# Kernel optimization log

Measured on AMD Instinct MI355X. Metric: run time of the kernel, lower is better.

The kernel has to match this reference:

```python
import jax, jax.numpy as jnp
import numpy as np

DIM = 768
NUM_HEADS = 8
HEAD_DIM = DIM // NUM_HEADS
SCALE = HEAD_DIM ** -0.5


def setup_inputs() -> dict:
    key = jax.random.key(0)
    k1, k2, k3, k4 = jax.random.split(key, 4)
    B, C, H, W = 8, DIM, 32, 32
    x = jax.random.normal(k1, (B, C, H, W), dtype=jnp.float32)
    # torch Linear stores weight as (out, in); y = x @ W.T + b
    w_qkv = jax.random.normal(k2, (3 * DIM, DIM), dtype=jnp.float32) * (DIM ** -0.5)
    w_proj = jax.random.normal(k3, (DIM, DIM), dtype=jnp.float32) * (DIM ** -0.5)
    b_proj = jax.random.normal(k4, (DIM,), dtype=jnp.float32) * 0.02
    return {"x": x, "w_qkv": w_qkv, "w_proj": w_proj, "b_proj": b_proj}


def reference(x, w_qkv, w_proj, b_proj):
    B, C, H, W = x.shape
    N = H * W
    nh, hd = NUM_HEADS, HEAD_DIM
    # (B, C, H, W) -> (B, N, C)
    tokens = x.reshape(B, C, N).transpose(0, 2, 1)
    qkv = tokens @ w_qkv.T  # (B, N, 3C), no bias (qkv_bias=False)
    qkv = qkv.reshape(B, N, 3, nh, hd).transpose(2, 0, 3, 1, 4)  # (3, B, nh, N, hd)
    q, k, v = qkv[0], qkv[1], qkv[2]
    attn = jnp.einsum('bhnd,bhmd->bhnm', q, k) * SCALE
    attn = jax.nn.softmax(attn, axis=-1)  # attn_drop=0.0 (eval)
    out = jnp.einsum('bhnm,bhmd->bhnd', attn, v)  # (B, nh, N, hd)
    out = out.transpose(0, 2, 1, 3).reshape(B, N, C)
    out = out @ w_proj.T + b_proj  # proj_drop=0.0
    return out.transpose(0, 2, 1).reshape(B, C, H, W)
```

## Files before the change

kernel.cpp:

```cpp
#include <hip/hip_runtime.h>

typedef short s16x8 __attribute__((ext_vector_type(8)));
typedef short s16x4 __attribute__((ext_vector_type(4)));
typedef float f32x4 __attribute__((ext_vector_type(4)));
typedef int   i32x4 __attribute__((ext_vector_type(4)));
typedef unsigned u32x2 __attribute__((ext_vector_type(2)));

#define SCALE_F 0.10206207261596577f
#define KLOG2E  0.14724444f
#define FIXM    12.0f

__device__ __forceinline__ unsigned short f2bf(float f) {
  unsigned u = __builtin_bit_cast(unsigned, f);
  u += 0x7fffu + ((u >> 16) & 1u);
  return (unsigned short)(u >> 16);
}
__device__ __forceinline__ unsigned cvt_pk_bf16(float a, float b) {
  unsigned r;
  asm("v_cvt_pk_bf16_f32 %0, %1, %2" : "=v"(r) : "v"(a), "v"(b));
  return r;
}
__device__ __forceinline__ float exp2_fast(float x) {
  float r;
  asm("v_exp_f32 %0, %1" : "=v"(r) : "v"(x));
  return r;
}

#define MFMA16(a, b, c) __builtin_amdgcn_mfma_f32_16x16x32_bf16((a), (b), (c), 0, 0, 0)

__device__ __forceinline__ void gl_lds16(const unsigned short* g, unsigned short* l) {
  __builtin_amdgcn_global_load_lds(
      (const __attribute__((address_space(1))) void*)g,
      (__attribute__((address_space(3))) void*)l, 16, 0, 0);
}

__global__ __launch_bounds__(256) void cvt_bf16_kernel(const float* __restrict__ src,
                                                       unsigned short* __restrict__ dst, int n4) {
  int i = blockIdx.x * 256 + threadIdx.x;
  if (i >= n4) return;
  f32x4 v = reinterpret_cast<const f32x4*>(src)[i];
  s16x4 o;
  o[0] = (short)f2bf(v[0]); o[1] = (short)f2bf(v[1]);
  o[2] = (short)f2bf(v[2]); o[3] = (short)f2bf(v[3]);
  reinterpret_cast<s16x4*>(dst)[i] = o;
}

__global__ __launch_bounds__(256) void transpose_x_kernel(const float* __restrict__ x,
                                                          unsigned short* __restrict__ tokens) {
  __shared__ float t[32][33];
  const int ct = blockIdx.x * 32, nt = blockIdx.y * 32, b = blockIdx.z;
  const int tx = threadIdx.x, ty = threadIdx.y;
  const float* xp = x + (size_t)b * 768 * 1024;
#pragma unroll
  for (int r = 0; r < 4; ++r) {
    int c = ty + r * 8;
    t[c][tx] = xp[(size_t)(ct + c) * 1024 + nt + tx];
  }
  __syncthreads();
  unsigned short* tp = tokens + (size_t)b * 1024 * 768;
#pragma unroll
  for (int r = 0; r < 4; ++r) {
    int n = ty + r * 8;
    tp[(size_t)(nt + n) * 768 + ct + tx] = f2bf(t[tx][n]);
  }
}

__global__ __launch_bounds__(512, 4) void qkv_gemm_kernel(const unsigned short* __restrict__ A,
                                                          const unsigned short* __restrict__ Bt,
                                                          unsigned short* __restrict__ Qo,
                                                          unsigned short* __restrict__ Ko,
                                                          unsigned short* __restrict__ Vt) {
  __shared__ unsigned short lds[36864];
  const int tid = threadIdx.x;
  const int wave = tid >> 6, lane = tid & 63;
  const int wm = wave >> 1, wn = wave & 1;
  const int lr = lane & 15, lg = lane >> 4;
  const int bid = blockIdx.x;
  const int xcd = bid & 7, idx = bid >> 3;
  const int m0 = (xcd * 4 + idx / 18) * 256;
  const int n0 = (idx % 18) * 128;

  const int srow = tid >> 2, sslot = tid & 3;

  f32x4 acc[4][4] = {};

#define STAGE_KT(ktv, bb)                                                       \
  {                                                                             \
    unsigned short* lb = lds + (bb) * 12288;                                    \
    _Pragma("unroll")                                                           \
    for (int rr = 0; rr < 2; ++rr) {                                            \
      const int row = rr * 128 + srow;                                          \
      const int c = sslot ^ ((row >> 1) & 3);                                   \
      gl_lds16(A + (size_t)(m0 + row) * 768 + (ktv) * 32 + c * 8,               \
               lb + rr * 4096 + wave * 512);                                    \
    }                                                                           \
    {                                                                           \
      const int c = sslot ^ ((srow >> 1) & 3);                                  \
      gl_lds16(Bt + (size_t)(n0 + srow) * 768 + (ktv) * 32 + c * 8,             \
               lb + 8192 + wave * 512);                                         \
    }                                                                           \
  }

  STAGE_KT(0, 0)
  STAGE_KT(1, 1)
  asm volatile("s_waitcnt vmcnt(3)" ::: "memory");
  __builtin_amdgcn_s_barrier();

  int cb = 0;
  for (int kt = 0; kt < 24; ++kt) {
    unsigned short* curb = lds + cb * 12288;
    if (kt < 22) {
      const int sb = (cb == 0) ? 2 : cb - 1;
      STAGE_KT(kt + 2, sb)
    }
    s16x8 af[4], bf[4];
#pragma unroll
    for (int mi = 0; mi < 4; ++mi) {
      const int row = wm * 64 + mi * 16 + lr;
      af[mi] = *reinterpret_cast<const s16x8*>(
          &curb[row * 32 + ((lg ^ ((row >> 1) & 3)) * 8)]);
    }
#pragma unroll
    for (int ni = 0; ni < 4; ++ni) {
      const int row = wn * 64 + ni * 16 + lr;
      bf[ni] = *reinterpret_cast<const s16x8*>(
          &curb[8192 + row * 32 + ((lg ^ ((row >> 1) & 3)) * 8)]);
    }
#pragma unroll
    for (int mi = 0; mi < 4; ++mi)
#pragma unroll
      for (int ni = 0; ni < 4; ++ni)
        acc[mi][ni] = MFMA16(af[mi], bf[ni], acc[mi][ni]);
    asm volatile("s_waitcnt lgkmcnt(0)" ::: "memory");
    if (kt < 22) {
      asm volatile("s_waitcnt vmcnt(3)" ::: "memory");
    } else if (kt == 22) {
      asm volatile("s_waitcnt vmcnt(0)" ::: "memory");
    }
    __builtin_amdgcn_s_barrier();
    cb = (cb == 2) ? 0 : cb + 1;
  }
#undef STAGE_KT

  const int colbase = n0 + wn * 64;
  const int ttype = colbase / 768;
  if (ttype == 2) {
#pragma unroll
    for (int ni = 0; ni < 4; ++ni) {
      const int cc = colbase + ni * 16 + lr - 2 * 768;
      const int h = cc / 96, d = cc - h * 96;
#pragma unroll
      for (int mi = 0; mi < 4; ++mi) {
        const int gm = m0 + wm * 64 + mi * 16 + lg * 4;
        const int b = gm >> 10, n = gm & 1023;
        const int np = (n & ~31) | (((n >> 2) & 3) << 3) | (((n >> 4) & 1) << 2);
        u32x2 p2;
        p2[0] = cvt_pk_bf16(acc[mi][ni][0], acc[mi][ni][1]);
        p2[1] = cvt_pk_bf16(acc[mi][ni][2], acc[mi][ni][3]);
        *reinterpret_cast<s16x4*>(Vt + ((size_t)(b * 8 + h) * 96 + d) * 1024 + np) =
            __builtin_bit_cast(s16x4, p2);
      }
    }
  } else {
    unsigned short* W = lds + wave * 4096;
    unsigned short* dstbuf = (ttype == 0) ? Qo : Ko;
#pragma unroll
    for (int mi = 0; mi < 4; ++mi)
#pragma unroll
      for (int ni = 0; ni < 4; ++ni) {
        const int cc = ni * 16 + lr;
        const int ch = cc >> 3, wi = cc & 7;
#pragma unroll
        for (int j = 0; j < 4; ++j) {
          const int r = mi * 16 + lg * 4 + j;
          W[r * 64 + ((ch ^ (r & 7)) * 8) + wi] = f2bf(acc[mi][ni][j]);
        }
      }
    asm volatile("s_waitcnt lgkmcnt(0)" ::: "memory");
    __builtin_amdgcn_sched_barrier(0);
#pragma unroll
    for (int i = 0; i < 8; ++i) {
      const int r = i * 8 + (lane >> 3), c = lane & 7;
      s16x8 v8 = *reinterpret_cast<const s16x8*>(&W[r * 64 + ((c ^ (r & 7)) * 8)]);
      const int cc = colbase + c * 8 - ttype * 768;
      const int h = cc / 96, d = cc - h * 96;
      const int gm = m0 + wm * 64 + r;
      const int b = gm >> 10, n = gm & 1023;
      *reinterpret_cast<s16x8*>(dstbuf + ((size_t)(b * 8 + h) * 1024 + n) * 96 + d) = v8;
    }
  }
}

__global__ __launch_bounds__(256, 4) void proj_gemm_kernel(const unsigned short* __restrict__ A,
                                                           const unsigned short* __restrict__ Bt,
                                                           const float* __restrict__ bias,
                                                           float* __restrict__ out) {
  __shared__ unsigned short lds[24576];
  const int tid = threadIdx.x;
  const int wave = tid >> 6, lane = tid & 63;
  const int wr = wave >> 1, wc = wave & 1;
  const int lr = lane & 15, lg = lane >> 4;
  const int bid = blockIdx.x;
  const int xcd = bid & 7, idx = bid >> 3;
  const int m0 = (xcd * 8 + idx / 6) * 128;
  const int n0 = (idx % 6) * 128;

  const int r2 = tid >> 2, ss = tid & 3;

  f32x4 acc[4][4] = {};

#define STAGE_P(ktv, bb)                                                        \
  {                                                                             \
    unsigned short* lb = lds + (bb) * 8192;                                     \
    _Pragma("unroll")                                                           \
    for (int i = 0; i < 2; ++i) {                                               \
      const int row = i * 64 + r2;                                              \
      const int c = ss ^ ((row >> 1) & 3);                                      \
      gl_lds16(A + (size_t)(m0 + row) * 768 + (ktv) * 32 + c * 8,               \
               lb + i * 2048 + wave * 512);                                     \
      gl_lds16(Bt + (size_t)(n0 + row) * 768 + (ktv) * 32 + c * 8,              \
               lb + 4096 + i * 2048 + wave * 512);                              \
    }                                                                           \
  }

  STAGE_P(0, 0)
  STAGE_P(1, 1)
  asm volatile("s_waitcnt vmcnt(4)" ::: "memory");
  __builtin_amdgcn_s_barrier();

  int cb = 0;
  for (int kt = 0; kt < 24; ++kt) {
    unsigned short* curb = lds + cb * 8192;
    if (kt < 22) {
      const int sb = (cb == 0) ? 2 : cb - 1;
      STAGE_P(kt + 2, sb)
    }
    s16x8 af[4], bf[4];
#pragma unroll
    for (int mi = 0; mi < 4; ++mi) {
      const int row = wr * 64 + mi * 16 + lr;
      af[mi] = *reinterpret_cast<const s16x8*>(
          &curb[row * 32 + ((lg ^ ((row >> 1) & 3)) * 8)]);
    }
#pragma unroll
    for (int ni = 0; ni < 4; ++ni) {
      const int row = wc * 64 + ni * 16 + lr;
      bf[ni] = *reinterpret_cast<const s16x8*>(
          &curb[4096 + row * 32 + ((lg ^ ((row >> 1) & 3)) * 8)]);
    }
#pragma unroll
    for (int mi = 0; mi < 4; ++mi)
#pragma unroll
      for (int ni = 0; ni < 4; ++ni)
        acc[mi][ni] = MFMA16(af[mi], bf[ni], acc[mi][ni]);
    asm volatile("s_waitcnt lgkmcnt(0)" ::: "memory");
    if (kt < 22) {
      asm volatile("s_waitcnt vmcnt(4)" ::: "memory");
    } else if (kt == 22) {
      asm volatile("s_waitcnt vmcnt(0)" ::: "memory");
    }
    __builtin_amdgcn_s_barrier();
    cb = (cb == 2) ? 0 : cb + 1;
  }
#undef STAGE_P

#pragma unroll
  for (int ni = 0; ni < 4; ++ni) {
    const int col = n0 + wc * 64 + ni * 16 + lr;
    const float bv = bias[col];
#pragma unroll
    for (int mi = 0; mi < 4; ++mi) {
      const int gm = m0 + wr * 64 + mi * 16 + lg * 4;
      const int b = gm >> 10, n = gm & 1023;
      f32x4 v;
#pragma unroll
      for (int j = 0; j < 4; ++j) v[j] = acc[mi][ni][j] + bv;
      *reinterpret_cast<f32x4*>(out + (size_t)b * 768 * 1024 + (size_t)col * 1024 + n) = v;
    }
  }
}

__global__ __launch_bounds__(256, 2) void attn_kernel(const unsigned short* __restrict__ Q,
                                                      const unsigned short* __restrict__ K,
                                                      const unsigned short* __restrict__ Vt,
                                                      unsigned short* __restrict__ Ao) {
  __shared__ unsigned short lds[3][12288];

  const int f = blockIdx.x;
  const int xcd = f & 7;
  const int g = (f >> 3) + xcd * 64;
  const int bh = g >> 3, qb = g & 7;

  const int tid = threadIdx.x, wave = tid >> 6, lane = tid & 63;
  const int lr = lane & 15, lg = lane >> 4;
  const int klo = (lr >> 1) & 3;

  const unsigned short* Qp = Q + (size_t)bh * 1024 * 96;
  const unsigned short* Kp = K + (size_t)bh * 1024 * 96;
  const unsigned short* Vp = Vt + (size_t)bh * 96 * 1024;

  s16x8 qreg[3][2];
#pragma unroll
  for (int u = 0; u < 2; ++u) {
    const int qrow = qb * 128 + wave * 32 + u * 16 + lr;
#pragma unroll
    for (int kd = 0; kd < 3; ++kd)
      qreg[kd][u] = *reinterpret_cast<const s16x8*>(Qp + (size_t)qrow * 96 + kd * 32 + lg * 8);
  }

  float l_lane[2] = {0.f, 0.f};
  f32x4 oacc[6][2] = {};

#define STAGE(bufi, kv0)                                                              \
  {                                                                                   \
    _Pragma("unroll")                                                                 \
    for (int i = 0; i < 6; ++i) {                                                     \
      const int wl = wave + 4 * i;                                                    \
      if (wl < 12) {                                                                  \
        const int kd = wl >> 2, rg = wl & 3;                                          \
        const int row = rg * 16 + (lane >> 2);                                        \
        const int c8 = (lane & 3) ^ ((row >> 1) & 3);                                 \
        gl_lds16(Kp + (size_t)((kv0) + row) * 96 + kd * 32 + c8 * 8,                  \
                 &lds[bufi][0] + kd * 2048 + rg * 512);                               \
      } else {                                                                        \
        const int v = wl - 12;                                                        \
        const int gs = v / 6, rg = v - gs * 6;                                        \
        const int drow = rg * 16 + (lane >> 2);                                       \
        const int c8 = (lane & 3) ^ ((drow >> 1) & 3);                                \
        gl_lds16(Vp + (size_t)drow * 1024 + (kv0) + gs * 32 + c8 * 8,                 \
                 &lds[bufi][0] + 6144 + gs * 3072 + rg * 512);                        \
      }                                                                               \
    }                                                                                 \
  }

  STAGE(0, 0);
  STAGE(1, 64);
  asm volatile("s_waitcnt vmcnt(6)" ::: "memory");
  __builtin_amdgcn_s_barrier();

  int buf = 0;
  for (int gt = 0; gt < 16; ++gt) {
    if (gt < 14) {
      const int sb = (buf == 0) ? 2 : buf - 1;
      STAGE(sb, (gt + 2) * 64);
    }

    f32x4 sacc[4][2] = {};
    __builtin_amdgcn_s_setprio(1);
#pragma unroll
    for (int c = 0; c < 4; ++c) {
      s16x8 kf[3];
#pragma unroll
      for (int kd = 0; kd < 3; ++kd)
        kf[kd] = *reinterpret_cast<const s16x8*>(
            &lds[buf][kd * 2048 + (c * 16 + lr) * 32 + ((lg ^ klo) * 8)]);
#pragma unroll
      for (int kd = 0; kd < 3; ++kd)
#pragma unroll
        for (int u = 0; u < 2; ++u)
          sacc[c][u] = MFMA16(kf[kd], qreg[kd][u], sacc[c][u]);
    }
    __builtin_amdgcn_s_setprio(0);

    unsigned pk[2][4][2];
#pragma unroll
    for (int u = 0; u < 2; ++u) {
      float ts = 0.f;
#pragma unroll
      for (int c = 0; c < 4; ++c) {
        float p0 = exp2_fast(__builtin_fmaf(sacc[c][u][0], KLOG2E, -FIXM));
        float p1 = exp2_fast(__builtin_fmaf(sacc[c][u][1], KLOG2E, -FIXM));
        float p2 = exp2_fast(__builtin_fmaf(sacc[c][u][2], KLOG2E, -FIXM));
        float p3 = exp2_fast(__builtin_fmaf(sacc[c][u][3], KLOG2E, -FIXM));
        ts += (p0 + p1) + (p2 + p3);
        pk[u][c][0] = cvt_pk_bf16(p0, p1);
        pk[u][c][1] = cvt_pk_bf16(p2, p3);
      }
      l_lane[u] += ts;
    }

    __builtin_amdgcn_s_setprio(1);
#pragma unroll
    for (int gs = 0; gs < 2; ++gs) {
      s16x8 pf[2];
#pragma unroll
      for (int u = 0; u < 2; ++u) {
        i32x4 bi;
        bi[0] = (int)pk[u][2 * gs][0];
        bi[1] = (int)pk[u][2 * gs][1];
        bi[2] = (int)pk[u][2 * gs + 1][0];
        bi[3] = (int)pk[u][2 * gs + 1][1];
        pf[u] = __builtin_bit_cast(s16x8, bi);
      }
#pragma unroll
      for (int dt = 0; dt < 6; ++dt) {
        s16x8 vf = *reinterpret_cast<const s16x8*>(
            &lds[buf][6144 + gs * 3072 + (dt * 16 + lr) * 32 + ((lg ^ klo) * 8)]);
#pragma unroll
        for (int u = 0; u < 2; ++u)
          oacc[dt][u] = MFMA16(vf, pf[u], oacc[dt][u]);
      }
    }
    __builtin_amdgcn_s_setprio(0);

    if (gt < 14) {
      asm volatile("s_waitcnt lgkmcnt(0)" ::: "memory");
      asm volatile("s_waitcnt vmcnt(6)" ::: "memory");
      __builtin_amdgcn_s_barrier();
    } else if (gt == 14) {
      asm volatile("s_waitcnt lgkmcnt(0)" ::: "memory");
      asm volatile("s_waitcnt vmcnt(0)" ::: "memory");
      __builtin_amdgcn_s_barrier();
    }
    buf = (buf == 2) ? 0 : buf + 1;
  }

  const int b_ = bh >> 3, h_ = bh & 7;
#pragma unroll
  for (int u = 0; u < 2; ++u) {
    float lt = l_lane[u];
    lt += __shfl_xor(lt, 16);
    lt += __shfl_xor(lt, 32);
    const float invl = 1.0f / lt;
    const int qrow = qb * 128 + wave * 32 + u * 16 + lr;
    unsigned short* orow = Ao + (size_t)(b_ * 1024 + qrow) * 768 + h_ * 96;
#pragma unroll
    for (int dt = 0; dt < 6; ++dt) {
      u32x2 p2;
      p2[0] = cvt_pk_bf16(oacc[dt][u][0] * invl, oacc[dt][u][1] * invl);
      p2[1] = cvt_pk_bf16(oacc[dt][u][2] * invl, oacc[dt][u][3] * invl);
      *reinterpret_cast<s16x4*>(orow + dt * 16 + lg * 4) = __builtin_bit_cast(s16x4, p2);
    }
  }
#undef STAGE
}

extern "C" void kernel_launch(void* const* d_in, const int* in_sizes, int n_in,
                              void* d_out, int out_size, void* d_ws, size_t ws_size,
                              hipStream_t stream) {
  const float* x = (const float*)d_in[0];
  const float* wqkv = (const float*)d_in[1];
  const float* wproj = (const float*)d_in[2];
  const float* bproj = (const float*)d_in[3];
  float* out = (float*)d_out;

  unsigned short* ws = (unsigned short*)d_ws;
  unsigned short* tokens = ws;
  unsigned short* wqkv_b = tokens + 8192 * 768;
  unsigned short* wproj_b = wqkv_b + 2304 * 768;
  unsigned short* Qb = wproj_b + 768 * 768;
  unsigned short* Kb = Qb + 64 * 1024 * 96;
  unsigned short* Vb = Kb + 64 * 1024 * 96;
  unsigned short* Ab = Vb + 64 * 1024 * 96;

  cvt_bf16_kernel<<<1728, 256, 0, stream>>>(wqkv, wqkv_b, 2304 * 768 / 4);
  cvt_bf16_kernel<<<576, 256, 0, stream>>>(wproj, wproj_b, 768 * 768 / 4);
  transpose_x_kernel<<<dim3(24, 32, 8), dim3(32, 8), 0, stream>>>(x, tokens);
  qkv_gemm_kernel<<<576, 512, 0, stream>>>(tokens, wqkv_b, Qb, Kb, Vb);
  attn_kernel<<<512, 256, 0, stream>>>(Qb, Kb, Vb, Ab);
  proj_gemm_kernel<<<384, 256, 0, stream>>>(Ab, wproj_b, bproj, out);
}
```

Before: 111.5 us.

## Halve attention query tile, double-buffer KV, merge weight casts, vectorize transpose

The attention kernel now gives each block 64 query rows (16 per wave) instead of 128, launching twice as many blocks. It also moves from triple to double buffering and raises occupancy to 3 blocks per CU. The two weight-conversion launches are merged into one kernel using packed bf16 conversion, and the input transpose now writes 16-byte vectors over 64-channel tiles. The smaller query tile halves reuse of each K/V tile loaded into LDS, and the shallower prefetch with full barriers exposes more load latency, in exchange for better occupancy and fewer launches.

Result: slower. 115.8 us (+3.9%).

```diff
diff --git a/kernel.cpp b/kernel.cpp
--- a/kernel.cpp
+++ b/kernel.cpp
@@ -34,35 +34,50 @@
       (__attribute__((address_space(3))) void*)l, 16, 0, 0);
 }
 
-__global__ __launch_bounds__(256) void cvt_bf16_kernel(const float* __restrict__ src,
-                                                       unsigned short* __restrict__ dst, int n4) {
+__global__ __launch_bounds__(256) void cvt2_bf16_kernel(const float* __restrict__ s0,
+                                                        unsigned short* __restrict__ d0, int n40,
+                                                        const float* __restrict__ s1,
+                                                        unsigned short* __restrict__ d1, int n41) {
   int i = blockIdx.x * 256 + threadIdx.x;
-  if (i >= n4) return;
+  const float* src;
+  unsigned short* dst;
+  if (i < n40) {
+    src = s0; dst = d0;
+  } else {
+    i -= n40;
+    if (i >= n41) return;
+    src = s1; dst = d1;
+  }
   f32x4 v = reinterpret_cast<const f32x4*>(src)[i];
-  s16x4 o;
-  o[0] = (short)f2bf(v[0]); o[1] = (short)f2bf(v[1]);
-  o[2] = (short)f2bf(v[2]); o[3] = (short)f2bf(v[3]);
-  reinterpret_cast<s16x4*>(dst)[i] = o;
+  u32x2 p;
+  p[0] = cvt_pk_bf16(v[0], v[1]);
+  p[1] = cvt_pk_bf16(v[2], v[3]);
+  reinterpret_cast<s16x4*>(dst)[i] = __builtin_bit_cast(s16x4, p);
 }
 
 __global__ __launch_bounds__(256) void transpose_x_kernel(const float* __restrict__ x,
                                                           unsigned short* __restrict__ tokens) {
-  __shared__ float t[32][33];
-  const int ct = blockIdx.x * 32, nt = blockIdx.y * 32, b = blockIdx.z;
-  const int tx = threadIdx.x, ty = threadIdx.y;
+  __shared__ float t[64][33];
+  const int ct = blockIdx.x * 64, nt = blockIdx.y * 32, b = blockIdx.z;
+  const int tid = threadIdx.x;
+  const int tx = tid & 31, ty = tid >> 5;
   const float* xp = x + (size_t)b * 768 * 1024;
 #pragma unroll
-  for (int r = 0; r < 4; ++r) {
-    int c = ty + r * 8;
+  for (int r = 0; r < 8; ++r) {
+    const int c = ty * 8 + r;
     t[c][tx] = xp[(size_t)(ct + c) * 1024 + nt + tx];
   }
   __syncthreads();
-  unsigned short* tp = tokens + (size_t)b * 1024 * 768;
-#pragma unroll
-  for (int r = 0; r < 4; ++r) {
-    int n = ty + r * 8;
-    tp[(size_t)(nt + n) * 768 + ct + tx] = f2bf(t[tx][n]);
-  }
+  const int n = tid >> 3, cg = tid & 7;
+  u32x2 lo, hi;
+  lo[0] = cvt_pk_bf16(t[cg * 8 + 0][n], t[cg * 8 + 1][n]);
+  lo[1] = cvt_pk_bf16(t[cg * 8 + 2][n], t[cg * 8 + 3][n]);
+  hi[0] = cvt_pk_bf16(t[cg * 8 + 4][n], t[cg * 8 + 5][n]);
+  hi[1] = cvt_pk_bf16(t[cg * 8 + 6][n], t[cg * 8 + 7][n]);
+  i32x4 v;
+  v[0] = (int)lo[0]; v[1] = (int)lo[1]; v[2] = (int)hi[0]; v[3] = (int)hi[1];
+  unsigned short* tp = tokens + (size_t)b * 1024 * 768 + (size_t)(nt + n) * 768 + ct + cg * 8;
+  *reinterpret_cast<i32x4*>(tp) = v;
 }
 
 __global__ __launch_bounds__(512, 4) void qkv_gemm_kernel(const unsigned short* __restrict__ A,
@@ -280,16 +295,16 @@
   }
 }
 
-__global__ __launch_bounds__(256, 2) void attn_kernel(const unsigned short* __restrict__ Q,
+__global__ __launch_bounds__(256, 3) void attn_kernel(const unsigned short* __restrict__ Q,
                                                       const unsigned short* __restrict__ K,
                                                       const unsigned short* __restrict__ Vt,
                                                       unsigned short* __restrict__ Ao) {
-  __shared__ unsigned short lds[3][12288];
+  __shared__ unsigned short lds[2][12288];
 
   const int f = blockIdx.x;
   const int xcd = f & 7;
-  const int g = (f >> 3) + xcd * 64;
-  const int bh = g >> 3, qb = g & 7;
+  const int g = (f >> 3) + xcd * 128;
+  const int bh = g >> 4, qb = g & 15;
 
   const int tid = threadIdx.x, wave = tid >> 6, lane = tid & 63;
   const int lr = lane & 15, lg = lane >> 4;
@@ -299,17 +314,14 @@
   const unsigned short* Kp = K + (size_t)bh * 1024 * 96;
   const unsigned short* Vp = Vt + (size_t)bh * 96 * 1024;
 
-  s16x8 qreg[3][2];
-#pragma unroll
-  for (int u = 0; u < 2; ++u) {
-    const int qrow = qb * 128 + wave * 32 + u * 16 + lr;
-#pragma unroll
-    for (int kd = 0; kd < 3; ++kd)
-      qreg[kd][u] = *reinterpret_cast<const s16x8*>(Qp + (size_t)qrow * 96 + kd * 32 + lg * 8);
-  }
-
-  float l_lane[2] = {0.f, 0.f};
-  f32x4 oacc[6][2] = {};
+  const int qrow = qb * 64 + wave * 16 + lr;
+  s16x8 qreg[3];
+#pragma unroll
+  for (int kd = 0; kd < 3; ++kd)
+    qreg[kd] = *reinterpret_cast<const s16x8*>(Qp + (size_t)qrow * 96 + kd * 32 + lg * 8);
+
+  float l_lane = 0.f;
+  f32x4 oacc[6] = {};
 
 #define STAGE(bufi, kv0)                                                              \
   {                                                                                   \
@@ -334,103 +346,73 @@
   }
 
   STAGE(0, 0);
-  STAGE(1, 64);
-  asm volatile("s_waitcnt vmcnt(6)" ::: "memory");
-  __builtin_amdgcn_s_barrier();
-
-  int buf = 0;
+  __syncthreads();
+
   for (int gt = 0; gt < 16; ++gt) {
-    if (gt < 14) {
-      const int sb = (buf == 0) ? 2 : buf - 1;
-      STAGE(sb, (gt + 2) * 64);
-    }
-
-    f32x4 sacc[4][2] = {};
+    const int buf = gt & 1;
+    if (gt < 15) STAGE(buf ^ 1, (gt + 1) * 64);
+
+    f32x4 sacc[4] = {};
     __builtin_amdgcn_s_setprio(1);
 #pragma unroll
     for (int c = 0; c < 4; ++c) {
-      s16x8 kf[3];
-#pragma unroll
-      for (int kd = 0; kd < 3; ++kd)
-        kf[kd] = *reinterpret_cast<const s16x8*>(
+#pragma unroll
+      for (int kd = 0; kd < 3; ++kd) {
+        s16x8 kf = *reinterpret_cast<const s16x8*>(
             &lds[buf][kd * 2048 + (c * 16 + lr) * 32 + ((lg ^ klo) * 8)]);
-#pragma unroll
-      for (int kd = 0; kd < 3; ++kd)
-#pragma unroll
-        for (int u = 0; u < 2; ++u)
-          sacc[c][u] = MFMA16(kf[kd], qreg[kd][u], sacc[c][u]);
+        sacc[c] = MFMA16(kf, qreg[kd], sacc[c]);
+      }
     }
     __builtin_amdgcn_s_setprio(0);
 
-    unsigned pk[2][4][2];
-#pragma unroll
-    for (int u = 0; u < 2; ++u) {
+    unsigned pk[4][2];
+    {
       float ts = 0.f;
 #pragma unroll
       for (int c = 0; c < 4; ++c) {
-        float p0 = exp2_fast(__builtin_fmaf(sacc[c][u][0], KLOG2E, -FIXM));
-        float p1 = exp2_fast(__builtin_fmaf(sacc[c][u][1], KLOG2E, -FIXM));
-        float p2 = exp2_fast(__builtin_fmaf(sacc[c][u][2], KLOG2E, -FIXM));
-        float p3 = exp2_fast(__builtin_fmaf(sacc[c][u][3], KLOG2E, -FIXM));
+        float p0 = exp2_fast(__builtin_fmaf(sacc[c][0], KLOG2E, -FIXM));
+        float p1 = exp2_fast(__builtin_fmaf(sacc[c][1], KLOG2E, -FIXM));
+        float p2 = exp2_fast(__builtin_fmaf(sacc[c][2], KLOG2E, -FIXM));
+        float p3 = exp2_fast(__builtin_fmaf(sacc[c][3], KLOG2E, -FIXM));
         ts += (p0 + p1) + (p2 + p3);
-        pk[u][c][0] = cvt_pk_bf16(p0, p1);
-        pk[u][c][1] = cvt_pk_bf16(p2, p3);
+        pk[c][0] = cvt_pk_bf16(p0, p1);
+        pk[c][1] = cvt_pk_bf16(p2, p3);
       }
-      l_lane[u] += ts;
+      l_lane += ts;
     }
 
     __builtin_amdgcn_s_setprio(1);
 #pragma unroll
     for (int gs = 0; gs < 2; ++gs) {
-      s16x8 pf[2];
-#pragma unroll
-      for (int u = 0; u < 2; ++u) {
-        i32x4 bi;
-        bi[0] = (int)pk[u][2 * gs][0];
-        bi[1] = (int)pk[u][2 * gs][1];
-        bi[2] = (int)pk[u][2 * gs + 1][0];
-        bi[3] = (int)pk[u][2 * gs + 1][1];
-        pf[u] = __builtin_bit_cast(s16x8, bi);
-      }
+      i32x4 bi;
+      bi[0] = (int)pk[2 * gs][0];
+      bi[1] = (int)pk[2 * gs][1];
+      bi[2] = (int)pk[2 * gs + 1][0];
+      bi[3] = (int)pk[2 * gs + 1][1];
+      s16x8 pf = __builtin_bit_cast(s16x8, bi);
 #pragma unroll
       for (int dt = 0; dt < 6; ++dt) {
         s16x8 vf = *reinterpret_cast<const s16x8*>(
             &lds[buf][6144 + gs * 3072 + (dt * 16 + lr) * 32 + ((lg ^ klo) * 8)]);
-#pragma unroll
-        for (int u = 0; u < 2; ++u)
-          oacc[dt][u] = MFMA16(vf, pf[u], oacc[dt][u]);
+        oacc[dt] = MFMA16(vf, pf, oacc[dt]);
       }
     }
     __builtin_amdgcn_s_setprio(0);
-
-    if (gt < 14) {
-      asm volatile("s_waitcnt lgkmcnt(0)" ::: "memory");
-      asm volatile("s_waitcnt vmcnt(6)" ::: "memory");
-      __builtin_amdgcn_s_barrier();
-    } else if (gt == 14) {
-      asm volatile("s_waitcnt lgkmcnt(0)" ::: "memory");
-      asm volatile("s_waitcnt vmcnt(0)" ::: "memory");
-      __builtin_amdgcn_s_barrier();
-    }
-    buf = (buf == 2) ? 0 : buf + 1;
-  }
-
+    __syncthreads();
+  }
+
+  float lt = l_lane;
+  lt += __shfl_xor(lt, 16);
+  lt += __shfl_xor(lt, 32);
+  const float invl = 1.0f / lt;
   const int b_ = bh >> 3, h_ = bh & 7;
-#pragma unroll
-  for (int u = 0; u < 2; ++u) {
-    float lt = l_lane[u];
-    lt += __shfl_xor(lt, 16);
-    lt += __shfl_xor(lt, 32);
-    const float invl = 1.0f / lt;
-    const int qrow = qb * 128 + wave * 32 + u * 16 + lr;
-    unsigned short* orow = Ao + (size_t)(b_ * 1024 + qrow) * 768 + h_ * 96;
-#pragma unroll
-    for (int dt = 0; dt < 6; ++dt) {
-      u32x2 p2;
-      p2[0] = cvt_pk_bf16(oacc[dt][u][0] * invl, oacc[dt][u][1] * invl);
-      p2[1] = cvt_pk_bf16(oacc[dt][u][2] * invl, oacc[dt][u][3] * invl);
-      *reinterpret_cast<s16x4*>(orow + dt * 16 + lg * 4) = __builtin_bit_cast(s16x4, p2);
-    }
+  unsigned short* orow = Ao + (size_t)(b_ * 1024 + qrow) * 768 + h_ * 96;
+#pragma unroll
+  for (int dt = 0; dt < 6; ++dt) {
+    u32x2 p2;
+    p2[0] = cvt_pk_bf16(oacc[dt][0] * invl, oacc[dt][1] * invl);
+    p2[1] = cvt_pk_bf16(oacc[dt][2] * invl, oacc[dt][3] * invl);
+    *reinterpret_cast<s16x4*>(orow + dt * 16 + lg * 4) = __builtin_bit_cast(s16x4, p2);
   }
 #undef STAGE
 }
@@ -453,10 +435,10 @@
   unsigned short* Vb = Kb + 64 * 1024 * 96;
   unsigned short* Ab = Vb + 64 * 1024 * 96;
 
-  cvt_bf16_kernel<<<1728, 256, 0, stream>>>(wqkv, wqkv_b, 2304 * 768 / 4);
-  cvt_bf16_kernel<<<576, 256, 0, stream>>>(wproj, wproj_b, 768 * 768 / 4);
-  transpose_x_kernel<<<dim3(24, 32, 8), dim3(32, 8), 0, stream>>>(x, tokens);
+  cvt2_bf16_kernel<<<2304, 256, 0, stream>>>(wqkv, wqkv_b, 2304 * 768 / 4,
+                                             wproj, wproj_b, 768 * 768 / 4);
+  transpose_x_kernel<<<dim3(12, 32, 8), 256, 0, stream>>>(x, tokens);
   qkv_gemm_kernel<<<576, 512, 0, stream>>>(tokens, wqkv_b, Qb, Kb, Vb);
-  attn_kernel<<<512, 256, 0, stream>>>(Qb, Kb, Vb, Ab);
+  attn_kernel<<<1024, 256, 0, stream>>>(Qb, Kb, Vb, Ab);
   proj_gemm_kernel<<<384, 256, 0, stream>>>(Ab, wproj_b, bproj, out);
 }
```

## Merge weight conversions, widen transpose stores, shrink QKV GEMM tiles to 128x128

Applied to the files above, without the earlier changes.

The two fp32-to-bf16 weight conversion launches are merged into one kernel that uses packed bf16 conversion. The transpose kernel now handles 64 channels per block and writes 16-byte vector stores instead of scattered 2-byte stores. The QKV GEMM moves from 256x128 tiles with 512 threads to 128x128 tiles with 256 threads, which doubles the grid to 1152 blocks and cuts LDS use for better occupancy and load balance, at the cost of less operand reuse per tile.

New measurement: 111.1 us. About the same (-0.4%).

```diff
diff --git a/kernel.cpp b/kernel.cpp
--- a/kernel.cpp
+++ b/kernel.cpp
@@ -34,97 +34,109 @@
       (__attribute__((address_space(3))) void*)l, 16, 0, 0);
 }
 
-__global__ __launch_bounds__(256) void cvt_bf16_kernel(const float* __restrict__ src,
-                                                       unsigned short* __restrict__ dst, int n4) {
+__global__ __launch_bounds__(256) void cvt2_bf16_kernel(const float* __restrict__ s0,
+                                                        unsigned short* __restrict__ d0, int n40,
+                                                        const float* __restrict__ s1,
+                                                        unsigned short* __restrict__ d1, int n41) {
   int i = blockIdx.x * 256 + threadIdx.x;
-  if (i >= n4) return;
+  const float* src;
+  unsigned short* dst;
+  if (i < n40) {
+    src = s0; dst = d0;
+  } else {
+    i -= n40;
+    if (i >= n41) return;
+    src = s1; dst = d1;
+  }
   f32x4 v = reinterpret_cast<const f32x4*>(src)[i];
-  s16x4 o;
-  o[0] = (short)f2bf(v[0]); o[1] = (short)f2bf(v[1]);
-  o[2] = (short)f2bf(v[2]); o[3] = (short)f2bf(v[3]);
-  reinterpret_cast<s16x4*>(dst)[i] = o;
+  u32x2 p;
+  p[0] = cvt_pk_bf16(v[0], v[1]);
+  p[1] = cvt_pk_bf16(v[2], v[3]);
+  reinterpret_cast<s16x4*>(dst)[i] = __builtin_bit_cast(s16x4, p);
 }
 
 __global__ __launch_bounds__(256) void transpose_x_kernel(const float* __restrict__ x,
                                                           unsigned short* __restrict__ tokens) {
-  __shared__ float t[32][33];
-  const int ct = blockIdx.x * 32, nt = blockIdx.y * 32, b = blockIdx.z;
-  const int tx = threadIdx.x, ty = threadIdx.y;
+  __shared__ float t[64][33];
+  const int ct = blockIdx.x * 64, nt = blockIdx.y * 32, b = blockIdx.z;
+  const int tid = threadIdx.x;
+  const int tx = tid & 31, ty = tid >> 5;
   const float* xp = x + (size_t)b * 768 * 1024;
 #pragma unroll
-  for (int r = 0; r < 4; ++r) {
-    int c = ty + r * 8;
+  for (int r = 0; r < 8; ++r) {
+    const int c = ty * 8 + r;
     t[c][tx] = xp[(size_t)(ct + c) * 1024 + nt + tx];
   }
   __syncthreads();
-  unsigned short* tp = tokens + (size_t)b * 1024 * 768;
-#pragma unroll
-  for (int r = 0; r < 4; ++r) {
-    int n = ty + r * 8;
-    tp[(size_t)(nt + n) * 768 + ct + tx] = f2bf(t[tx][n]);
-  }
-}
-
-__global__ __launch_bounds__(512, 4) void qkv_gemm_kernel(const unsigned short* __restrict__ A,
+  const int n = tid >> 3, cg = tid & 7;
+  u32x2 lo, hi;
+  lo[0] = cvt_pk_bf16(t[cg * 8 + 0][n], t[cg * 8 + 1][n]);
+  lo[1] = cvt_pk_bf16(t[cg * 8 + 2][n], t[cg * 8 + 3][n]);
+  hi[0] = cvt_pk_bf16(t[cg * 8 + 4][n], t[cg * 8 + 5][n]);
+  hi[1] = cvt_pk_bf16(t[cg * 8 + 6][n], t[cg * 8 + 7][n]);
+  i32x4 v;
+  v[0] = (int)lo[0]; v[1] = (int)lo[1]; v[2] = (int)hi[0]; v[3] = (int)hi[1];
+  unsigned short* tp = tokens + (size_t)b * 1024 * 768 + (size_t)(nt + n) * 768 + ct + cg * 8;
+  *reinterpret_cast<i32x4*>(tp) = v;
+}
+
+__global__ __launch_bounds__(256, 4) void qkv_gemm_kernel(const unsigned short* __restrict__ A,
                                                           const unsigned short* __restrict__ Bt,
                                                           unsigned short* __restrict__ Qo,
                                                           unsigned short* __restrict__ Ko,
                                                           unsigned short* __restrict__ Vt) {
-  __shared__ unsigned short lds[36864];
+  __shared__ unsigned short lds[24576];
   const int tid = threadIdx.x;
   const int wave = tid >> 6, lane = tid & 63;
-  const int wm = wave >> 1, wn = wave & 1;
+  const int wr = wave >> 1, wc = wave & 1;
   const int lr = lane & 15, lg = lane >> 4;
   const int bid = blockIdx.x;
   const int xcd = bid & 7, idx = bid >> 3;
-  const int m0 = (xcd * 4 + idx / 18) * 256;
+  const int m0 = (xcd * 8 + idx / 18) * 128;
   const int n0 = (idx % 18) * 128;
 
-  const int srow = tid >> 2, sslot = tid & 3;
+  const int r2 = tid >> 2, ss = tid & 3;
 
   f32x4 acc[4][4] = {};
 
-#define STAGE_KT(ktv, bb)                                                       \
+#define STAGE_Q(ktv, bb)                                                        \
   {                                                                             \
-    unsigned short* lb = lds + (bb) * 12288;                                    \
+    unsigned short* lb = lds + (bb) * 8192;                                     \
     _Pragma("unroll")                                                           \
-    for (int rr = 0; rr < 2; ++rr) {                                            \
-      const int row = rr * 128 + srow;                                          \
-      const int c = sslot ^ ((row >> 1) & 3);                                   \
+    for (int i = 0; i < 2; ++i) {                                               \
+      const int row = i * 64 + r2;                                              \
+      const int c = ss ^ ((row >> 1) & 3);                                      \
       gl_lds16(A + (size_t)(m0 + row) * 768 + (ktv) * 32 + c * 8,               \
-               lb + rr * 4096 + wave * 512);                                    \
+               lb + i * 2048 + wave * 512);                                     \
+      gl_lds16(Bt + (size_t)(n0 + row) * 768 + (ktv) * 32 + c * 8,              \
+               lb + 4096 + i * 2048 + wave * 512);                              \
     }                                                                           \
-    {                                                                           \
-      const int c = sslot ^ ((srow >> 1) & 3);                                  \
-      gl_lds16(Bt + (size_t)(n0 + srow) * 768 + (ktv) * 32 + c * 8,             \
-               lb + 8192 + wave * 512);                                         \
-    }                                                                           \
-  }
-
-  STAGE_KT(0, 0)
-  STAGE_KT(1, 1)
-  asm volatile("s_waitcnt vmcnt(3)" ::: "memory");
+  }
+
+  STAGE_Q(0, 0)
+  STAGE_Q(1, 1)
+  asm volatile("s_waitcnt vmcnt(4)" ::: "memory");
   __builtin_amdgcn_s_barrier();
 
   int cb = 0;
   for (int kt = 0; kt < 24; ++kt) {
-    unsigned short* curb = lds + cb * 12288;
+    unsigned short* curb = lds + cb * 8192;
     if (kt < 22) {
       const int sb = (cb == 0) ? 2 : cb - 1;
-      STAGE_KT(kt + 2, sb)
+      STAGE_Q(kt + 2, sb)
     }
     s16x8 af[4], bf[4];
 #pragma unroll
     for (int mi = 0; mi < 4; ++mi) {
-      const int row = wm * 64 + mi * 16 + lr;
+      const int row = wr * 64 + mi * 16 + lr;
       af[mi] = *reinterpret_cast<const s16x8*>(
           &curb[row * 32 + ((lg ^ ((row >> 1) & 3)) * 8)]);
     }
 #pragma unroll
     for (int ni = 0; ni < 4; ++ni) {
-      const int row = wn * 64 + ni * 16 + lr;
+      const int row = wc * 64 + ni * 16 + lr;
       bf[ni] = *reinterpret_cast<const s16x8*>(
-          &curb[8192 + row * 32 + ((lg ^ ((row >> 1) & 3)) * 8)]);
+          &curb[4096 + row * 32 + ((lg ^ ((row >> 1) & 3)) * 8)]);
     }
 #pragma unroll
     for (int mi = 0; mi < 4; ++mi)
@@ -133,16 +145,16 @@
         acc[mi][ni] = MFMA16(af[mi], bf[ni], acc[mi][ni]);
     asm volatile("s_waitcnt lgkmcnt(0)" ::: "memory");
     if (kt < 22) {
-      asm volatile("s_waitcnt vmcnt(3)" ::: "memory");
+      asm volatile("s_waitcnt vmcnt(4)" ::: "memory");
     } else if (kt == 22) {
       asm volatile("s_waitcnt vmcnt(0)" ::: "memory");
     }
     __builtin_amdgcn_s_barrier();
     cb = (cb == 2) ? 0 : cb + 1;
   }
-#undef STAGE_KT
-
-  const int colbase = n0 + wn * 64;
+#undef STAGE_Q
+
+  const int colbase = n0 + wc * 64;
   const int ttype = colbase / 768;
   if (ttype == 2) {
 #pragma unroll
@@ -151,7 +163,7 @@
       const int h = cc / 96, d = cc - h * 96;
 #pragma unroll
       for (int mi = 0; mi < 4; ++mi) {
-        const int gm = m0 + wm * 64 + mi * 16 + lg * 4;
+        const int gm = m0 + wr * 64 + mi * 16 + lg * 4;
         const int b = gm >> 10, n = gm & 1023;
         const int np = (n & ~31) | (((n >> 2) & 3) << 3) | (((n >> 4) & 1) << 2);
         u32x2 p2;
@@ -184,7 +196,7 @@
       s16x8 v8 = *reinterpret_cast<const s16x8*>(&W[r * 64 + ((c ^ (r & 7)) * 8)]);
       const int cc = colbase + c * 8 - ttype * 768;
       const int h = cc / 96, d = cc - h * 96;
-      const int gm = m0 + wm * 64 + r;
+      const int gm = m0 + wr * 64 + r;
       const int b = gm >> 10, n = gm & 1023;
       *reinterpret_cast<s16x8*>(dstbuf + ((size_t)(b * 8 + h) * 1024 + n) * 96 + d) = v8;
     }
@@ -453,10 +465,10 @@
   unsigned short* Vb = Kb + 64 * 1024 * 96;
   unsigned short* Ab = Vb + 64 * 1024 * 96;
 
-  cvt_bf16_kernel<<<1728, 256, 0, stream>>>(wqkv, wqkv_b, 2304 * 768 / 4);
-  cvt_bf16_kernel<<<576, 256, 0, stream>>>(wproj, wproj_b, 768 * 768 / 4);
-  transpose_x_kernel<<<dim3(24, 32, 8), dim3(32, 8), 0, stream>>>(x, tokens);
-  qkv_gemm_kernel<<<576, 512, 0, stream>>>(tokens, wqkv_b, Qb, Kb, Vb);
+  cvt2_bf16_kernel<<<2304, 256, 0, stream>>>(wqkv, wqkv_b, 2304 * 768 / 4,
+                                             wproj, wproj_b, 768 * 768 / 4);
+  transpose_x_kernel<<<dim3(12, 32, 8), 256, 0, stream>>>(x, tokens);
+  qkv_gemm_kernel<<<1152, 256, 0, stream>>>(tokens, wqkv_b, Qb, Kb, Vb);
   attn_kernel<<<512, 256, 0, stream>>>(Qb, Kb, Vb, Ab);
   proj_gemm_kernel<<<384, 256, 0, stream>>>(Ab, wproj_b, bproj, out);
 }
```
